# Kernel tuning notes

Measured on AMD Instinct MI355X. Metric: run time of the kernel, lower is better.

## Reference

```python
import jax, jax.numpy as jnp
import numpy as np

B, S, FEAT, DK = 128, 2048, 512, 64

def setup_inputs() -> dict:
    key = jax.random.key(0)
    k1, k2, k3, k4, k5 = jax.random.split(key, 5)
    input_k = jax.random.normal(k1, (B, S, FEAT), dtype=jnp.float32)
    input_q = jax.random.normal(k2, (B, FEAT), dtype=jnp.float32)
    context_len = jax.random.randint(k3, (B,), 0, S + 1, dtype=jnp.int32)
    # Linear weights stored as [in, out] so y = x @ W
    W_K = jax.random.normal(k4, (FEAT, DK), dtype=jnp.float32) / np.sqrt(FEAT)
    W_Q = jax.random.normal(k5, (FEAT, DK), dtype=jnp.float32) / np.sqrt(FEAT)
    return {"input_k": input_k, "input_q": input_q, "context_len": context_len,
            "W_K": W_K, "W_Q": W_Q}

def reference(input_k, input_q, context_len, W_K, W_Q):
    # K: [B,S,dk], q: [B,dk]
    K = jnp.einsum('bsf,fd->bsd', input_k, W_K)
    q = input_q @ W_Q
    scores = jnp.einsum('bd,bsd->bs', q, K)  # [B,S] (n_heads=1, no scaling in original)
    mask = jnp.arange(S)[None, :] < context_len[:, None]  # [B,S]
    attn = jax.nn.softmax(jnp.where(mask, scores, -1e30), axis=-1)  # [B,S]
    context = jnp.einsum('bs,bsf->bf', attn, input_k)  # [B,FEAT]
    # length==0 rows produce zeros in the original
    context = jnp.where((context_len > 0)[:, None], context, 0.0)
    return context
```

## Files before the change

kernel.cpp:

```cpp
#include <hip/hip_runtime.h>
#include <math.h>

#define B_    128
#define S_    2048
#define FEAT_ 512
#define DK_   64
#define NSPLIT 32
#define CHUNK  (S_ / NSPLIT)

__global__ __launch_bounds__(256) void qv_kernel(
    const float* __restrict__ input_q, const float* __restrict__ W_Q,
    const float* __restrict__ W_K, float* __restrict__ v) {
  int b = blockIdx.x;
  int tid = threadIdx.x;
  __shared__ float xq[FEAT_];
  __shared__ float part[4][DK_];
  __shared__ float qs[DK_];
  for (int f = tid; f < FEAT_; f += 256) xq[f] = input_q[b * FEAT_ + f];
  __syncthreads();
  {
    int d = tid & 63, c = tid >> 6;
    float s = 0.f;
    int f0 = c * 128;
    for (int f = f0; f < f0 + 128; ++f) s = fmaf(xq[f], W_Q[f * DK_ + d], s);
    part[c][d] = s;
  }
  __syncthreads();
  if (tid < DK_)
    qs[tid] = part[0][tid] + part[1][tid] + part[2][tid] + part[3][tid];
  __syncthreads();
  for (int f = tid; f < FEAT_; f += 256) {
    const float4* wk = (const float4*)(W_K + f * DK_);
    float s = 0.f;
#pragma unroll
    for (int d4 = 0; d4 < DK_ / 4; ++d4) {
      float4 w = wk[d4];
      s = fmaf(w.x, qs[d4 * 4 + 0], s);
      s = fmaf(w.y, qs[d4 * 4 + 1], s);
      s = fmaf(w.z, qs[d4 * 4 + 2], s);
      s = fmaf(w.w, qs[d4 * 4 + 3], s);
    }
    v[b * FEAT_ + f] = s;
  }
}

__device__ __forceinline__ float dot8(float4 x0, float4 x1, float4 v0, float4 v1) {
  float p = x0.x * v0.x;
  p = fmaf(x0.y, v0.y, p);
  p = fmaf(x0.z, v0.z, p);
  p = fmaf(x0.w, v0.w, p);
  p = fmaf(x1.x, v1.x, p);
  p = fmaf(x1.y, v1.y, p);
  p = fmaf(x1.z, v1.z, p);
  p = fmaf(x1.w, v1.w, p);
  return p;
}

__global__ __launch_bounds__(256) void pass_kernel(
    const float* __restrict__ input_k, const int* __restrict__ ctx,
    const float* __restrict__ v, float* __restrict__ pm,
    float* __restrict__ pl, float* __restrict__ pacc) {
  int split = blockIdx.x;
  int b = blockIdx.y;
  int L = ctx[b];
  int s0 = split * CHUNK;
  int s1 = min(s0 + CHUNK, L);
  int tid = threadIdx.x, wave = tid >> 6, lane = tid & 63;

  const float* vb = v + b * FEAT_;
  float4 v0 = *(const float4*)(vb + lane * 4);
  float4 v1 = *(const float4*)(vb + 256 + lane * 4);

  float m = -INFINITY, l = 0.f;
  float4 a0 = make_float4(0.f, 0.f, 0.f, 0.f);
  float4 a1 = make_float4(0.f, 0.f, 0.f, 0.f);

  const float* base = input_k + (size_t)b * S_ * FEAT_;
  int s = s0 + wave;

  for (; s + 12 < s1; s += 16) {
    const float* r0 = base + (size_t)s * FEAT_;
    const float* r1 = r0 + 4 * FEAT_;
    const float* r2 = r0 + 8 * FEAT_;
    const float* r3 = r0 + 12 * FEAT_;
    float4 x00 = *(const float4*)(r0 + lane * 4);
    float4 x01 = *(const float4*)(r0 + 256 + lane * 4);
    float4 x10 = *(const float4*)(r1 + lane * 4);
    float4 x11 = *(const float4*)(r1 + 256 + lane * 4);
    float4 x20 = *(const float4*)(r2 + lane * 4);
    float4 x21 = *(const float4*)(r2 + 256 + lane * 4);
    float4 x30 = *(const float4*)(r3 + lane * 4);
    float4 x31 = *(const float4*)(r3 + 256 + lane * 4);

    float p0 = dot8(x00, x01, v0, v1);
    float p1 = dot8(x10, x11, v0, v1);
    float p2 = dot8(x20, x21, v0, v1);
    float p3 = dot8(x30, x31, v0, v1);
#pragma unroll
    for (int off = 32; off; off >>= 1) {
      p0 += __shfl_xor(p0, off, 64);
      p1 += __shfl_xor(p1, off, 64);
      p2 += __shfl_xor(p2, off, 64);
      p3 += __shfl_xor(p3, off, 64);
    }
    float mn = fmaxf(fmaxf(fmaxf(p0, p1), fmaxf(p2, p3)), m);
    float sc = __expf(m - mn);
    float w0 = __expf(p0 - mn), w1 = __expf(p1 - mn);
    float w2 = __expf(p2 - mn), w3 = __expf(p3 - mn);
    l = fmaf(l, sc, (w0 + w1) + (w2 + w3));
#define ACC(comp, f0c, f1c, f2c, f3c)                       \
    {                                                        \
      float t = comp * sc;                                   \
      t = fmaf(w0, f0c, t);                                  \
      t = fmaf(w1, f1c, t);                                  \
      t = fmaf(w2, f2c, t);                                  \
      t = fmaf(w3, f3c, t);                                  \
      comp = t;                                              \
    }
    ACC(a0.x, x00.x, x10.x, x20.x, x30.x)
    ACC(a0.y, x00.y, x10.y, x20.y, x30.y)
    ACC(a0.z, x00.z, x10.z, x20.z, x30.z)
    ACC(a0.w, x00.w, x10.w, x20.w, x30.w)
    ACC(a1.x, x01.x, x11.x, x21.x, x31.x)
    ACC(a1.y, x01.y, x11.y, x21.y, x31.y)
    ACC(a1.z, x01.z, x11.z, x21.z, x31.z)
    ACC(a1.w, x01.w, x11.w, x21.w, x31.w)
#undef ACC
    m = mn;
  }

  for (; s < s1; s += 4) {
    const float* row = base + (size_t)s * FEAT_;
    float4 x0 = *(const float4*)(row + lane * 4);
    float4 x1 = *(const float4*)(row + 256 + lane * 4);
    float p = dot8(x0, x1, v0, v1);
#pragma unroll
    for (int off = 32; off; off >>= 1) p += __shfl_xor(p, off, 64);
    float mn = fmaxf(m, p);
    float sc = __expf(m - mn);
    float w = __expf(p - mn);
    l = fmaf(l, sc, w);
    a0.x = fmaf(w, x0.x, a0.x * sc);
    a0.y = fmaf(w, x0.y, a0.y * sc);
    a0.z = fmaf(w, x0.z, a0.z * sc);
    a0.w = fmaf(w, x0.w, a0.w * sc);
    a1.x = fmaf(w, x1.x, a1.x * sc);
    a1.y = fmaf(w, x1.y, a1.y * sc);
    a1.z = fmaf(w, x1.z, a1.z * sc);
    a1.w = fmaf(w, x1.w, a1.w * sc);
    m = mn;
  }

  __shared__ float sm[4], sl[4];
  __shared__ float sa[4][FEAT_];
  if (lane == 0) { sm[wave] = m; sl[wave] = l; }
  *(float4*)&sa[wave][lane * 4] = a0;
  *(float4*)&sa[wave][256 + lane * 4] = a1;
  __syncthreads();

  float M = fmaxf(fmaxf(sm[0], sm[1]), fmaxf(sm[2], sm[3]));
  int idx = b * NSPLIT + split;
  if (M == -INFINITY) {
    if (tid == 0) { pm[idx] = -INFINITY; pl[idx] = 0.f; }
    for (int f = tid; f < FEAT_; f += 256) pacc[(size_t)idx * FEAT_ + f] = 0.f;
    return;
  }
  float e0 = __expf(sm[0] - M), e1 = __expf(sm[1] - M);
  float e2 = __expf(sm[2] - M), e3 = __expf(sm[3] - M);
  if (tid == 0) {
    pm[idx] = M;
    pl[idx] = e0 * sl[0] + e1 * sl[1] + e2 * sl[2] + e3 * sl[3];
  }
  for (int f = tid; f < FEAT_; f += 256)
    pacc[(size_t)idx * FEAT_ + f] =
        e0 * sa[0][f] + e1 * sa[1][f] + e2 * sa[2][f] + e3 * sa[3][f];
}

__global__ __launch_bounds__(256) void combine_kernel(
    const float* __restrict__ pm, const float* __restrict__ pl,
    const float* __restrict__ pacc, float* __restrict__ out) {
  int b = blockIdx.x;
  int tid = threadIdx.x;
  __shared__ float e[NSPLIT];
  __shared__ float inv_s;
  if (tid < NSPLIT) {
    float mi = pm[b * NSPLIT + tid];
    float M = mi;
#pragma unroll
    for (int off = 16; off; off >>= 1) M = fmaxf(M, __shfl_xor(M, off, 64));
    float ei = (M == -INFINITY) ? 0.f : __expf(mi - M);
    e[tid] = ei;
    float lw = ei * pl[b * NSPLIT + tid];
#pragma unroll
    for (int off = 16; off; off >>= 1) lw += __shfl_xor(lw, off, 64);
    if (tid == 0) inv_s = (lw > 0.f) ? 1.f / lw : 0.f;
  }
  __syncthreads();
  float inv = inv_s;
  for (int f = tid; f < FEAT_; f += 256) {
    float s = 0.f;
#pragma unroll
    for (int i = 0; i < NSPLIT; ++i)
      s = fmaf(e[i], pacc[((size_t)(b * NSPLIT + i)) * FEAT_ + f], s);
    out[b * FEAT_ + f] = s * inv;
  }
}

extern "C" void kernel_launch(void* const* d_in, const int* in_sizes, int n_in,
                              void* d_out, int out_size, void* d_ws, size_t ws_size,
                              hipStream_t stream) {
  const float* input_k = (const float*)d_in[0];
  const float* input_q = (const float*)d_in[1];
  const int*   ctx     = (const int*)d_in[2];
  const float* W_K     = (const float*)d_in[3];
  const float* W_Q     = (const float*)d_in[4];
  float* out = (float*)d_out;

  char* ws = (char*)d_ws;
  float* v    = (float*)ws;
  float* pm   = (float*)(ws + (size_t)B_ * FEAT_ * sizeof(float));
  float* pl   = pm + B_ * NSPLIT;
  float* pacc = pl + B_ * NSPLIT;

  qv_kernel<<<B_, 256, 0, stream>>>(input_q, W_Q, W_K, v);
  pass_kernel<<<dim3(NSPLIT, B_), 256, 0, stream>>>(input_k, ctx, v, pm, pl, pacc);
  combine_kernel<<<B_, 256, 0, stream>>>(pm, pl, pacc, out);
}
```

Before: 66.06 us.

## Double-buffer full-chunk loads with inline asm and skip empty splits

For splits that are fully inside the context length, the pass kernel now issues global loads through inline assembly in a two-deep register double buffer with explicit vmcnt waits, so loads for the next group of rows overlap the softmax and accumulate work on the current group. Splits that start past the context length exit early and write only the max and sum, without zero-filling the partial accumulator. The combine kernel skips splits whose weight is zero, so it never reads those unwritten accumulators. The hand-scheduled asm and sched barriers raise register pressure and depend on exact vmcnt counting.

```diff
diff --git a/kernel.cpp b/kernel.cpp
--- a/kernel.cpp
+++ b/kernel.cpp
@@ -7,6 +7,78 @@
 #define DK_   64
 #define NSPLIT 32
 #define CHUNK  (S_ / NSPLIT)
+
+typedef float f32x4 __attribute__((ext_vector_type(4)));
+
+#define SBAR() __builtin_amdgcn_sched_barrier(0)
+
+__device__ __forceinline__ void ld4(f32x4& d, const float* p) {
+  asm volatile("global_load_dwordx4 %0, %1, off" : "=v"(d) : "v"(p) : "memory");
+}
+__device__ __forceinline__ void ld4o(f32x4& d, const float* p) {
+  asm volatile("global_load_dwordx4 %0, %1, off offset:1024"
+               : "=v"(d) : "v"(p) : "memory");
+}
+#define VWAIT(N)                                              \
+  do {                                                        \
+    asm volatile("s_waitcnt vmcnt(" #N ")" ::: "memory");     \
+    SBAR();                                                   \
+  } while (0)
+
+#define ISSUE4(d0, d1, d2, d3, d4, d5, d6, d7, srow)                \
+  do {                                                              \
+    const float* r_ = base + (size_t)(srow) * FEAT_ + lane * 4;     \
+    ld4(d0, r_);              ld4o(d1, r_);                         \
+    ld4(d2, r_ + 4 * FEAT_);  ld4o(d3, r_ + 4 * FEAT_);             \
+    ld4(d4, r_ + 8 * FEAT_);  ld4o(d5, r_ + 8 * FEAT_);             \
+    ld4(d6, r_ + 12 * FEAT_); ld4o(d7, r_ + 12 * FEAT_);            \
+    SBAR();                                                         \
+  } while (0)
+
+__device__ __forceinline__ float dot8(f32x4 x0, f32x4 x1, f32x4 v0, f32x4 v1) {
+  float p = x0[0] * v0[0];
+  p = fmaf(x0[1], v0[1], p);
+  p = fmaf(x0[2], v0[2], p);
+  p = fmaf(x0[3], v0[3], p);
+  p = fmaf(x1[0], v1[0], p);
+  p = fmaf(x1[1], v1[1], p);
+  p = fmaf(x1[2], v1[2], p);
+  p = fmaf(x1[3], v1[3], p);
+  return p;
+}
+
+__device__ __forceinline__ float wredsum(float p) {
+#pragma unroll
+  for (int off = 32; off; off >>= 1) p += __shfl_xor(p, off, 64);
+  return p;
+}
+
+__device__ __forceinline__ void compute4(
+    f32x4 x0, f32x4 x1, f32x4 x2, f32x4 x3,
+    f32x4 x4, f32x4 x5, f32x4 x6, f32x4 x7,
+    f32x4 v0, f32x4 v1, float& m, float& l, f32x4& a0, f32x4& a1) {
+  float p0 = dot8(x0, x1, v0, v1);
+  float p1 = dot8(x2, x3, v0, v1);
+  float p2 = dot8(x4, x5, v0, v1);
+  float p3 = dot8(x6, x7, v0, v1);
+  p0 = wredsum(p0);
+  p1 = wredsum(p1);
+  p2 = wredsum(p2);
+  p3 = wredsum(p3);
+  float mn = fmaxf(fmaxf(fmaxf(p0, p1), fmaxf(p2, p3)), m);
+  float sc = __expf(m - mn);
+  float w0 = __expf(p0 - mn), w1 = __expf(p1 - mn);
+  float w2 = __expf(p2 - mn), w3 = __expf(p3 - mn);
+  l = fmaf(l, sc, (w0 + w1) + (w2 + w3));
+#pragma unroll
+  for (int j = 0; j < 4; ++j) {
+    a0[j] = fmaf(w0, x0[j],
+            fmaf(w1, x2[j], fmaf(w2, x4[j], fmaf(w3, x6[j], a0[j] * sc))));
+    a1[j] = fmaf(w0, x1[j],
+            fmaf(w1, x3[j], fmaf(w2, x5[j], fmaf(w3, x7[j], a1[j] * sc))));
+  }
+  m = mn;
+}
 
 __global__ __launch_bounds__(256) void qv_kernel(
     const float* __restrict__ input_q, const float* __restrict__ W_Q,
@@ -30,30 +102,18 @@
     qs[tid] = part[0][tid] + part[1][tid] + part[2][tid] + part[3][tid];
   __syncthreads();
   for (int f = tid; f < FEAT_; f += 256) {
-    const float4* wk = (const float4*)(W_K + f * DK_);
+    const f32x4* wk = (const f32x4*)(W_K + f * DK_);
     float s = 0.f;
 #pragma unroll
     for (int d4 = 0; d4 < DK_ / 4; ++d4) {
-      float4 w = wk[d4];
-      s = fmaf(w.x, qs[d4 * 4 + 0], s);
-      s = fmaf(w.y, qs[d4 * 4 + 1], s);
-      s = fmaf(w.z, qs[d4 * 4 + 2], s);
-      s = fmaf(w.w, qs[d4 * 4 + 3], s);
+      f32x4 w = wk[d4];
+      s = fmaf(w[0], qs[d4 * 4 + 0], s);
+      s = fmaf(w[1], qs[d4 * 4 + 1], s);
+      s = fmaf(w[2], qs[d4 * 4 + 2], s);
+      s = fmaf(w[3], qs[d4 * 4 + 3], s);
     }
     v[b * FEAT_ + f] = s;
   }
-}
-
-__device__ __forceinline__ float dot8(float4 x0, float4 x1, float4 v0, float4 v1) {
-  float p = x0.x * v0.x;
-  p = fmaf(x0.y, v0.y, p);
-  p = fmaf(x0.z, v0.z, p);
-  p = fmaf(x0.w, v0.w, p);
-  p = fmaf(x1.x, v1.x, p);
-  p = fmaf(x1.y, v1.y, p);
-  p = fmaf(x1.z, v1.z, p);
-  p = fmaf(x1.w, v1.w, p);
-  return p;
 }
 
 __global__ __launch_bounds__(256) void pass_kernel(
@@ -64,107 +124,83 @@
   int b = blockIdx.y;
   int L = ctx[b];
   int s0 = split * CHUNK;
-  int s1 = min(s0 + CHUNK, L);
   int tid = threadIdx.x, wave = tid >> 6, lane = tid & 63;
-
-  const float* vb = v + b * FEAT_;
-  float4 v0 = *(const float4*)(vb + lane * 4);
-  float4 v1 = *(const float4*)(vb + 256 + lane * 4);
+  int idx = b * NSPLIT + split;
+
+  if (s0 >= L) {
+    if (tid == 0) { pm[idx] = -INFINITY; pl[idx] = 0.f; }
+    return;
+  }
+
+  const float* vb = v + b * FEAT_ + lane * 4;
+  f32x4 v0, v1;
+  ld4(v0, vb);
+  ld4o(v1, vb);
+  VWAIT(0);
 
   float m = -INFINITY, l = 0.f;
-  float4 a0 = make_float4(0.f, 0.f, 0.f, 0.f);
-  float4 a1 = make_float4(0.f, 0.f, 0.f, 0.f);
+  f32x4 a0 = {0.f, 0.f, 0.f, 0.f};
+  f32x4 a1 = {0.f, 0.f, 0.f, 0.f};
 
   const float* base = input_k + (size_t)b * S_ * FEAT_;
-  int s = s0 + wave;
-
-  for (; s + 12 < s1; s += 16) {
-    const float* r0 = base + (size_t)s * FEAT_;
-    const float* r1 = r0 + 4 * FEAT_;
-    const float* r2 = r0 + 8 * FEAT_;
-    const float* r3 = r0 + 12 * FEAT_;
-    float4 x00 = *(const float4*)(r0 + lane * 4);
-    float4 x01 = *(const float4*)(r0 + 256 + lane * 4);
-    float4 x10 = *(const float4*)(r1 + lane * 4);
-    float4 x11 = *(const float4*)(r1 + 256 + lane * 4);
-    float4 x20 = *(const float4*)(r2 + lane * 4);
-    float4 x21 = *(const float4*)(r2 + 256 + lane * 4);
-    float4 x30 = *(const float4*)(r3 + lane * 4);
-    float4 x31 = *(const float4*)(r3 + 256 + lane * 4);
-
-    float p0 = dot8(x00, x01, v0, v1);
-    float p1 = dot8(x10, x11, v0, v1);
-    float p2 = dot8(x20, x21, v0, v1);
-    float p3 = dot8(x30, x31, v0, v1);
-#pragma unroll
-    for (int off = 32; off; off >>= 1) {
-      p0 += __shfl_xor(p0, off, 64);
-      p1 += __shfl_xor(p1, off, 64);
-      p2 += __shfl_xor(p2, off, 64);
-      p3 += __shfl_xor(p3, off, 64);
+  int sb = s0 + wave;
+
+  if (L >= s0 + CHUNK) {
+    f32x4 c0, c1, c2, c3, c4, c5, c6, c7;
+    f32x4 n0, n1, n2, n3, n4, n5, n6, n7;
+    ISSUE4(c0, c1, c2, c3, c4, c5, c6, c7, sb);
+    ISSUE4(n0, n1, n2, n3, n4, n5, n6, n7, sb + 16);
+    VWAIT(8);
+    compute4(c0, c1, c2, c3, c4, c5, c6, c7, v0, v1, m, l, a0, a1);
+    ISSUE4(c0, c1, c2, c3, c4, c5, c6, c7, sb + 32);
+    VWAIT(8);
+    compute4(n0, n1, n2, n3, n4, n5, n6, n7, v0, v1, m, l, a0, a1);
+    ISSUE4(n0, n1, n2, n3, n4, n5, n6, n7, sb + 48);
+    VWAIT(8);
+    compute4(c0, c1, c2, c3, c4, c5, c6, c7, v0, v1, m, l, a0, a1);
+    VWAIT(0);
+    compute4(n0, n1, n2, n3, n4, n5, n6, n7, v0, v1, m, l, a0, a1);
+  } else {
+    int s1 = L;
+    int s = sb;
+    for (; s + 12 < s1; s += 16) {
+      const float* r_ = base + (size_t)s * FEAT_ + lane * 4;
+      f32x4 x0 = *(const f32x4*)(r_);
+      f32x4 x1 = *(const f32x4*)(r_ + 256);
+      f32x4 x2 = *(const f32x4*)(r_ + 4 * FEAT_);
+      f32x4 x3 = *(const f32x4*)(r_ + 4 * FEAT_ + 256);
+      f32x4 x4 = *(const f32x4*)(r_ + 8 * FEAT_);
+      f32x4 x5 = *(const f32x4*)(r_ + 8 * FEAT_ + 256);
+      f32x4 x6 = *(const f32x4*)(r_ + 12 * FEAT_);
+      f32x4 x7 = *(const f32x4*)(r_ + 12 * FEAT_ + 256);
+      compute4(x0, x1, x2, x3, x4, x5, x6, x7, v0, v1, m, l, a0, a1);
     }
-    float mn = fmaxf(fmaxf(fmaxf(p0, p1), fmaxf(p2, p3)), m);
-    float sc = __expf(m - mn);
-    float w0 = __expf(p0 - mn), w1 = __expf(p1 - mn);
-    float w2 = __expf(p2 - mn), w3 = __expf(p3 - mn);
-    l = fmaf(l, sc, (w0 + w1) + (w2 + w3));
-#define ACC(comp, f0c, f1c, f2c, f3c)                       \
-    {                                                        \
-      float t = comp * sc;                                   \
-      t = fmaf(w0, f0c, t);                                  \
-      t = fmaf(w1, f1c, t);                                  \
-      t = fmaf(w2, f2c, t);                                  \
-      t = fmaf(w3, f3c, t);                                  \
-      comp = t;                                              \
+    for (; s < s1; s += 4) {
+      const float* r_ = base + (size_t)s * FEAT_ + lane * 4;
+      f32x4 x0 = *(const f32x4*)(r_);
+      f32x4 x1 = *(const f32x4*)(r_ + 256);
+      float p = wredsum(dot8(x0, x1, v0, v1));
+      float mn = fmaxf(m, p);
+      float sc = __expf(m - mn);
+      float w = __expf(p - mn);
+      l = fmaf(l, sc, w);
+#pragma unroll
+      for (int j = 0; j < 4; ++j) {
+        a0[j] = fmaf(w, x0[j], a0[j] * sc);
+        a1[j] = fmaf(w, x1[j], a1[j] * sc);
+      }
+      m = mn;
     }
-    ACC(a0.x, x00.x, x10.x, x20.x, x30.x)
-    ACC(a0.y, x00.y, x10.y, x20.y, x30.y)
-    ACC(a0.z, x00.z, x10.z, x20.z, x30.z)
-    ACC(a0.w, x00.w, x10.w, x20.w, x30.w)
-    ACC(a1.x, x01.x, x11.x, x21.x, x31.x)
-    ACC(a1.y, x01.y, x11.y, x21.y, x31.y)
-    ACC(a1.z, x01.z, x11.z, x21.z, x31.z)
-    ACC(a1.w, x01.w, x11.w, x21.w, x31.w)
-#undef ACC
-    m = mn;
-  }
-
-  for (; s < s1; s += 4) {
-    const float* row = base + (size_t)s * FEAT_;
-    float4 x0 = *(const float4*)(row + lane * 4);
-    float4 x1 = *(const float4*)(row + 256 + lane * 4);
-    float p = dot8(x0, x1, v0, v1);
-#pragma unroll
-    for (int off = 32; off; off >>= 1) p += __shfl_xor(p, off, 64);
-    float mn = fmaxf(m, p);
-    float sc = __expf(m - mn);
-    float w = __expf(p - mn);
-    l = fmaf(l, sc, w);
-    a0.x = fmaf(w, x0.x, a0.x * sc);
-    a0.y = fmaf(w, x0.y, a0.y * sc);
-    a0.z = fmaf(w, x0.z, a0.z * sc);
-    a0.w = fmaf(w, x0.w, a0.w * sc);
-    a1.x = fmaf(w, x1.x, a1.x * sc);
-    a1.y = fmaf(w, x1.y, a1.y * sc);
-    a1.z = fmaf(w, x1.z, a1.z * sc);
-    a1.w = fmaf(w, x1.w, a1.w * sc);
-    m = mn;
   }
 
   __shared__ float sm[4], sl[4];
   __shared__ float sa[4][FEAT_];
   if (lane == 0) { sm[wave] = m; sl[wave] = l; }
-  *(float4*)&sa[wave][lane * 4] = a0;
-  *(float4*)&sa[wave][256 + lane * 4] = a1;
+  *(f32x4*)&sa[wave][lane * 4] = a0;
+  *(f32x4*)&sa[wave][256 + lane * 4] = a1;
   __syncthreads();
 
   float M = fmaxf(fmaxf(sm[0], sm[1]), fmaxf(sm[2], sm[3]));
-  int idx = b * NSPLIT + split;
-  if (M == -INFINITY) {
-    if (tid == 0) { pm[idx] = -INFINITY; pl[idx] = 0.f; }
-    for (int f = tid; f < FEAT_; f += 256) pacc[(size_t)idx * FEAT_ + f] = 0.f;
-    return;
-  }
   float e0 = __expf(sm[0] - M), e1 = __expf(sm[1] - M);
   float e2 = __expf(sm[2] - M), e3 = __expf(sm[3] - M);
   if (tid == 0) {
@@ -199,9 +235,9 @@
   float inv = inv_s;
   for (int f = tid; f < FEAT_; f += 256) {
     float s = 0.f;
-#pragma unroll
     for (int i = 0; i < NSPLIT; ++i)
-      s = fmaf(e[i], pacc[((size_t)(b * NSPLIT + i)) * FEAT_ + f], s);
+      if (e[i] > 0.f)
+        s = fmaf(e[i], pacc[((size_t)(b * NSPLIT + i)) * FEAT_ + f], s);
     out[b * FEAT_ + f] = s * inv;
   }
 }
```

After: 76.06 us. 15.1% more time.
